# Performance work log

Hardware: AMD Instinct MI355X
Metric: run time of the kernel (lower is better)

## Reference

```python
import jax, jax.numpy as jnp
import numpy as np

L, B, T, V, E, H = 6, 4, 1024, 32000, 768, 12
D = E // H  # head_size = 64


def setup_inputs() -> dict:
    key = jax.random.key(0)
    ks = jax.random.split(key, 12)
    s = 0.02
    n = lambda k, shape: jax.random.normal(k, shape, jnp.float32) * s
    return {
        "idx": jax.random.randint(ks[0], (B, T), 0, V),
        "tok_emb": n(ks[1], (V, E)),
        "pos_emb": n(ks[2], (T, E)),
        "ln1_w": jnp.ones((L, E)), "ln1_b": jnp.zeros((L, E)),
        "wq": n(ks[3], (L, E, H, D)),
        "wk": n(ks[4], (L, E, H, D)),
        "wv": n(ks[5], (L, E, H, D)),
        "wo": n(ks[6], (L, E, E)), "bo": jnp.zeros((L, E)),
        "ln2_w": jnp.ones((L, E)), "ln2_b": jnp.zeros((L, E)),
        "w1": n(ks[7], (L, E, 4 * E)), "b1": jnp.zeros((L, 4 * E)),
        "w2": n(ks[8], (L, 4 * E, E)), "b2": jnp.zeros((L, E)),
        "lnf_w": jnp.ones((E,)), "lnf_b": jnp.zeros((E,)),
        "head_w": n(ks[9], (E, V)), "head_b": jnp.zeros((V,)),
    }


def _ln(x, w, b, eps=1e-5):
    m = x.mean(-1, keepdims=True)
    v = ((x - m) ** 2).mean(-1, keepdims=True)
    return (x - m) * jax.lax.rsqrt(v + eps) * w + b


def _forward(idx, tok_emb, pos_emb, ln1_w, ln1_b, wq, wk, wv, wo, bo,
             ln2_w, ln2_b, w1, b1, w2, b2, lnf_w, lnf_b, head_w, head_b):
    t = idx.shape[1]
    x = tok_emb[idx] + pos_emb[None, :t]          # [B,T,E]
    causal = jnp.tril(jnp.ones((t, t), bool))     # tril buffer
    scale = jnp.asarray(D, x.dtype) ** -0.5       # k.shape[-1] ** -0.5

    def block(x, p):
        l1w, l1b, Wq, Wk, Wv, Wo, Bo, l2w, l2b, W1, B1, W2, B2 = p
        h = _ln(x, l1w, l1b)
        q = jnp.einsum('btc,chd->bthd', h, Wq)
        k = jnp.einsum('btc,chd->bthd', h, Wk)
        v = jnp.einsum('btc,chd->bthd', h, Wv)
        wei = jnp.einsum('bqhd,bkhd->bhqk', q, k) * scale
        wei = jnp.where(causal, wei, -jnp.inf)
        wei = jax.nn.softmax(wei, axis=-1)
        att = jnp.einsum('bhqk,bkhd->bqhd', wei, v).reshape(x.shape)
        x = x + (att @ Wo + Bo)
        h2 = _ln(x, l2w, l2b)
        x = x + (jax.nn.relu(h2 @ W1 + B1) @ W2 + B2)
        return x, None

    params = (ln1_w, ln1_b, wq, wk, wv, wo, bo, ln2_w, ln2_b, w1, b1, w2, b2)
    x, _ = jax.lax.scan(block, x, params)
    x = _ln(x, lnf_w, lnf_b)
    return x @ head_w + head_b                    # [B,T,V] logits


def reference(idx, tok_emb, pos_emb, ln1_w, ln1_b, wq, wk, wv, wo, bo,
              ln2_w, ln2_b, w1, b1, w2, b2, lnf_w, lnf_b, head_w, head_b):
    return _forward(idx, tok_emb, pos_emb, ln1_w, ln1_b, wq, wk, wv, wo, bo,
                    ln2_w, ln2_b, w1, b1, w2, b2, lnf_w, lnf_b, head_w, head_b)
```

## Files before the change

kernel.cpp:

```cpp
#include <hip/hip_runtime.h>
#include <hip/hip_bf16.h>
#include <math.h>

#define L_LAYERS 6
#define BB 4
#define TT 1024
#define VV 32000
#define EE 768
#define HH 12
#define DD 64
#define BT (BB * TT)

typedef unsigned short u16;
typedef unsigned int   u32;
typedef __attribute__((ext_vector_type(8))) short short8;
typedef __attribute__((ext_vector_type(8))) unsigned short ushort8v;
typedef __attribute__((ext_vector_type(4))) unsigned short ushort4v;
typedef __attribute__((ext_vector_type(4))) float f32x4;

__device__ __forceinline__ float b2f_lo(u32 u) { union { u32 i; float f; } c; c.i = u << 16;          return c.f; }
__device__ __forceinline__ float b2f_hi(u32 u) { union { u32 i; float f; } c; c.i = u & 0xffff0000u;  return c.f; }
__device__ __forceinline__ u16  f2b(float f)   { union { float f; u32 i; } c{f}; u32 r = c.i + 0x7fffu + ((c.i >> 16) & 1u); return (u16)(r >> 16); }

__device__ __forceinline__ void gload16(const void* g, void* l) {
    __builtin_amdgcn_global_load_lds(
        (const __attribute__((address_space(1))) void*)g,
        (__attribute__((address_space(3))) void*)l, 16, 0, 0);
}

__global__ __launch_bounds__(256) void embed_kernel(
    const int* __restrict__ idx, const float* __restrict__ tok_emb,
    const float* __restrict__ pos_emb, float* __restrict__ x)
{
    int i = blockIdx.x * 256 + threadIdx.x;
    int e  = i % EE;
    int bt = i / EE;
    int t  = bt % TT;
    int tok = idx[bt];
    x[i] = tok_emb[(size_t)tok * EE + e] + pos_emb[(size_t)t * EE + e];
}

__global__ __launch_bounds__(256) void ln_kernel(
    const float* __restrict__ X, const float* __restrict__ w,
    const float* __restrict__ b, u16* __restrict__ Y)
{
    const int lane = threadIdx.x & 63;
    const size_t row = blockIdx.x * 4 + (threadIdx.x >> 6);
    const float* x = X + row * EE;

    f32x4 v[3];
    #pragma unroll
    for (int k = 0; k < 3; k++)
        v[k] = *(const f32x4*)&x[lane * 4 + k * 256];

    float s = 0.0f;
    #pragma unroll
    for (int k = 0; k < 3; k++) s += v[k][0] + v[k][1] + v[k][2] + v[k][3];
    #pragma unroll
    for (int off = 32; off; off >>= 1) s += __shfl_xor(s, off);
    const float mean = s * (1.0f / EE);

    float q = 0.0f;
    #pragma unroll
    for (int k = 0; k < 3; k++)
        #pragma unroll
        for (int j = 0; j < 4; j++) {
            v[k][j] -= mean;
            q += v[k][j] * v[k][j];
        }
    #pragma unroll
    for (int off = 32; off; off >>= 1) q += __shfl_xor(q, off);
    const float rstd = rsqrtf(q * (1.0f / EE) + 1e-5f);

    u16* y = Y + row * EE;
    #pragma unroll
    for (int k = 0; k < 3; k++) {
        const f32x4 wv = *(const f32x4*)&w[lane * 4 + k * 256];
        const f32x4 bv = *(const f32x4*)&b[lane * 4 + k * 256];
        ushort4v o;
        #pragma unroll
        for (int j = 0; j < 4; j++) o[j] = f2b(v[k][j] * rstd * wv[j] + bv[j]);
        *(ushort4v*)&y[lane * 4 + k * 256] = o;
    }
}

__device__ __forceinline__ void transpose_tile(
    const float* __restrict__ W, u16* __restrict__ Wt,
    int K, int N, int kt, int nt)
{
    __shared__ float t[32][33];
    const int k0 = kt * 32;
    const int n0 = nt * 32;
    const int c = threadIdx.x & 31;
    const int r = threadIdx.x >> 5;
    #pragma unroll
    for (int i = 0; i < 4; i++)
        t[r + i * 8][c] = W[(size_t)(k0 + r + i * 8) * N + n0 + c];
    __syncthreads();
    #pragma unroll
    for (int i = 0; i < 4; i++) {
        int rr = r + i * 8;
        Wt[(size_t)(n0 + rr) * K + k0 + c] = f2b(t[c][rr]);
    }
}

__global__ __launch_bounds__(256) void transpose_cvt(
    const float* __restrict__ W, u16* __restrict__ Wt, int K, int N)
{
    transpose_tile(W, Wt, K, N, blockIdx.y, blockIdx.x);
}

__global__ __launch_bounds__(256) void transpose_layer(
    const float* __restrict__ wq, const float* __restrict__ wk,
    const float* __restrict__ wv, const float* __restrict__ wo,
    const float* __restrict__ w1, const float* __restrict__ w2,
    u16* __restrict__ wt)
{
    const int t = blockIdx.x;
    if (t < 2304) {
        const int m = t / 576, r = t % 576;
        const float* Ws[4] = {wq, wk, wv, wo};
        transpose_tile(Ws[m], wt + (size_t)m * 768 * 768, 768, 768, r / 24, r % 24);
    } else if (t < 4608) {
        const int r = t - 2304;
        transpose_tile(w1, wt + (size_t)4 * 768 * 768, 768, 3072, r / 96, r % 96);
    } else {
        const int r = t - 4608;
        transpose_tile(w2, wt + (size_t)4 * 768 * 768 + (size_t)3072 * 768,
                       3072, 768, r / 24, r % 24);
    }
}

template<int RELU, int RES, int OUTBF, int MFRAG>
__global__ __launch_bounds__(256) void gemm_bf16(
    const u16* __restrict__ A, const u16* __restrict__ Bt,
    const float* __restrict__ bias, const float* __restrict__ res,
    void* __restrict__ Cv, int M, int N, int K)
{
    constexpr int TM = MFRAG * 32;
    __shared__ u16 As[TM * 64];
    __shared__ u16 Bs[128 * 64];

    const int tid  = threadIdx.x;
    const int lane = tid & 63;
    const int w    = tid >> 6;
    const int wr   = w >> 1, wc = w & 1;
    const int m0 = blockIdx.x * TM;
    const int n0 = blockIdx.y * 128;

    const int cs = (lane & 7) ^ (lane >> 3);
    const int rl = lane >> 3;

    int aoff[2 * MFRAG], boff[8];
    const int kq = lane >> 4;
    #pragma unroll
    for (int mi = 0; mi < MFRAG; mi++) {
        int rg = wr * (MFRAG * 16) + mi * 16 + (lane & 15);
        #pragma unroll
        for (int ks = 0; ks < 2; ks++)
            aoff[2 * mi + ks] = rg * 64 + (((ks * 4 + kq) ^ (rg & 7)) * 8);
    }
    #pragma unroll
    for (int ni = 0; ni < 4; ni++) {
        int rg = wc * 64 + ni * 16 + (lane & 15);
        #pragma unroll
        for (int ks = 0; ks < 2; ks++)
            boff[2 * ni + ks] = rg * 64 + (((ks * 4 + kq) ^ (rg & 7)) * 8);
    }

    f32x4 acc[MFRAG][4] = {};

    for (int k0 = 0; k0 < K; k0 += 64) {
        __syncthreads();
        #pragma unroll
        for (int i = 0; i < MFRAG; i++) {
            const int seg = i * 4 + w;
            const int row = seg * 8 + rl;
            gload16(A + (size_t)(m0 + row) * K + k0 + cs * 8, &As[seg * 512]);
        }
        #pragma unroll
        for (int i = 0; i < 4; i++) {
            const int seg = i * 4 + w;
            const int row = seg * 8 + rl;
            gload16(Bt + (size_t)(n0 + row) * K + k0 + cs * 8, &Bs[seg * 512]);
        }
        __syncthreads();
        #pragma unroll
        for (int ks = 0; ks < 2; ks++) {
            short8 af[MFRAG], bfv[4];
            #pragma unroll
            for (int mi = 0; mi < MFRAG; mi++) af[mi] = *(const short8*)&As[aoff[2 * mi + ks]];
            #pragma unroll
            for (int ni = 0; ni < 4; ni++) bfv[ni] = *(const short8*)&Bs[boff[2 * ni + ks]];
            #pragma unroll
            for (int mi = 0; mi < MFRAG; mi++)
                #pragma unroll
                for (int ni = 0; ni < 4; ni++)
                    acc[mi][ni] = __builtin_amdgcn_mfma_f32_16x16x32_bf16(
                        af[mi], bfv[ni], acc[mi][ni], 0, 0, 0);
        }
    }

    const int rbase = m0 + wr * (MFRAG * 16) + (lane >> 4) * 4;
    const int cbase = n0 + wc * 64 + (lane & 15);
    #pragma unroll
    for (int ni = 0; ni < 4; ni++) {
        const int c = cbase + ni * 16;
        const float bv = bias ? bias[c] : 0.0f;
        #pragma unroll
        for (int mi = 0; mi < MFRAG; mi++) {
            const int r = rbase + mi * 16;
            #pragma unroll
            for (int i = 0; i < 4; i++) {
                float v = acc[mi][ni][i] + bv;
                const size_t off = (size_t)(r + i) * N + c;
                if (RES)  v += res[off];
                if (RELU) v = fmaxf(v, 0.0f);
                if (OUTBF) ((u16*)Cv)[off] = f2b(v);
                else       ((float*)Cv)[off] = v;
            }
        }
    }
}

#define AST 72
__global__ __launch_bounds__(256) void attn_mfma(
    const u16* __restrict__ qkv, u16* __restrict__ O)
{
    const int tid = threadIdx.x;
    const int qi = blockIdx.x;
    const int h  = blockIdx.y;
    const int b  = blockIdx.z;
    const int q0 = qi * 64;

    __shared__ u16 Ks[2][64 * 64];
    __shared__ u16 Vt[2][80 * AST];
    __shared__ u16 Ps[64 * AST];

    const int lane = tid & 63;
    const int w    = tid >> 6;
    const int lr   = lane & 15;
    const int lk   = lane >> 4;

    const int cs = (lane & 7) ^ (lane >> 3);
    const int rl = lane >> 3;
    const int vk2 = tid & 31;
    const int vdc = tid >> 5;

    for (int i = tid; i < 16 * AST; i += 256) {
        const int r = i / AST, c = i % AST;
        const u16 v = (r == 0) ? (u16)0x3F80 : (u16)0;
        Vt[0][(64 + r) * AST + c] = v;
        Vt[1][(64 + r) * AST + c] = v;
    }

    {
        const int sr = tid >> 2, sc = tid & 3;
        const u16* src = qkv + (size_t)(b * TT + q0 + sr) * 2304 + h * 64 + sc * 16;
        *(ushort8v*)&Ps[sr * AST + sc * 16]     = *(const ushort8v*)src;
        *(ushort8v*)&Ps[sr * AST + sc * 16 + 8] = *(const ushort8v*)(src + 8);
    }
    __syncthreads();
    short8 aq[2];
    #pragma unroll
    for (int ks = 0; ks < 2; ks++)
        aq[ks] = *(const short8*)&Ps[(w * 16 + lr) * AST + lk * 8 + ks * 32];

    ushort8v vr0, vr1;
    auto K_ISSUE = [&](int t, int bf) {
        const int k0 = t * 64;
        #pragma unroll
        for (int j = 0; j < 2; ++j) {
            const int seg = j * 4 + w;
            const int row = seg * 8 + rl;
            gload16(qkv + (size_t)(b * TT + k0 + row) * 2304 + 768 + h * 64 + cs * 8,
                    &Ks[bf][seg * 512]);
        }
    };
    auto V_LOAD = [&](int t) {
        const int k0 = t * 64;
        const u16* p = qkv + (size_t)(b * TT + k0 + 2 * vk2) * 2304 + 1536 + h * 64 + vdc * 8;
        vr0 = *(const ushort8v*)p;
        vr1 = *(const ushort8v*)(p + 2304);
    };
    auto V_WRITE = [&](int bf) {
        #pragma unroll
        for (int j = 0; j < 8; ++j) {
            const u32 val = (u32)vr0[j] | ((u32)vr1[j] << 16);
            *(u32*)&Vt[bf][(vdc * 8 + j) * AST + 2 * vk2] = val;
        }
    };

    K_ISSUE(0, 0);
    V_LOAD(0);
    V_WRITE(0);
    __syncthreads();

    f32x4 oacc[5] = {};
    float m_run[4];
    #pragma unroll
    for (int i = 0; i < 4; i++) m_run[i] = -3.0e38f;

    const int qrow = q0 + w * 16 + lk * 4;
    const float SC = 0.18033688f;

    for (int t = 0; t <= qi; ++t) {
        const int cur = t & 1;

        f32x4 sfrag[4] = {};
        #pragma unroll
        for (int ks = 0; ks < 2; ks++)
            #pragma unroll
            for (int nt = 0; nt < 4; nt++) {
                const int rg = nt * 16 + lr;
                short8 bk = *(const short8*)&Ks[cur][rg * 64 + (((ks * 4 + lk) ^ (rg & 7)) * 8)];
                sfrag[nt] = __builtin_amdgcn_mfma_f32_16x16x32_bf16(aq[ks], bk, sfrag[nt], 0, 0, 0);
            }

        if (t < qi) { K_ISSUE(t + 1, cur ^ 1); V_LOAD(t + 1); }

        const int k0 = t * 64;
        float sv[4][4], mxv[4];
        float need = 0.0f;
        #pragma unroll
        for (int i = 0; i < 4; i++) {
            float mx = -3.0e38f;
            #pragma unroll
            for (int nt = 0; nt < 4; nt++) {
                float s = sfrag[nt][i] * SC;
                if (t == qi && (k0 + nt * 16 + lr) > (qrow + i)) s = -3.0e38f;
                sv[i][nt] = s;
                mx = fmaxf(mx, s);
            }
            mx = fmaxf(mx, __shfl_xor(mx, 1));
            mx = fmaxf(mx, __shfl_xor(mx, 2));
            mx = fmaxf(mx, __shfl_xor(mx, 4));
            mx = fmaxf(mx, __shfl_xor(mx, 8));
            mxv[i] = mx;
            need = fmaxf(need, mx - m_run[i]);
        }
        if (!__all(need <= 11.5f)) {
            #pragma unroll
            for (int i = 0; i < 4; i++) {
                const float m_new = fmaxf(m_run[i], mxv[i]);
                const float scale = exp2f(m_run[i] - m_new);
                #pragma unroll
                for (int dt = 0; dt < 5; dt++) oacc[dt][i] *= scale;
                m_run[i] = m_new;
            }
        }
        #pragma unroll
        for (int i = 0; i < 4; i++)
            #pragma unroll
            for (int nt = 0; nt < 4; nt++)
                sv[i][nt] = exp2f(sv[i][nt] - m_run[i]);

        #pragma unroll
        for (int i = 0; i < 4; i++)
            #pragma unroll
            for (int nt = 0; nt < 4; nt++)
                Ps[(w * 16 + lk * 4 + i) * AST + nt * 16 + lr] = f2b(sv[i][nt]);

        #pragma unroll
        for (int ks = 0; ks < 2; ks++) {
            short8 ap = *(const short8*)&Ps[(w * 16 + lr) * AST + lk * 8 + ks * 32];
            #pragma unroll
            for (int dt = 0; dt < 5; dt++) {
                short8 bv = *(const short8*)&Vt[cur][(dt * 16 + lr) * AST + lk * 8 + ks * 32];
                oacc[dt] = __builtin_amdgcn_mfma_f32_16x16x32_bf16(ap, bv, oacc[dt], 0, 0, 0);
            }
        }

        if (t < qi) V_WRITE(cur ^ 1);
        __syncthreads();
    }

    #pragma unroll
    for (int i = 0; i < 4; i++) {
        const float li  = __shfl(oacc[4][i], lane & 48);
        const float inv = 1.0f / li;
        u16* dst = O + (size_t)(b * TT + q0 + w * 16 + lk * 4 + i) * 768 + h * 64 + lr;
        #pragma unroll
        for (int dt = 0; dt < 4; dt++)
            dst[dt * 16] = f2b(oacc[dt][i] * inv);
    }
}

extern "C" void kernel_launch(void* const* d_in, const int* in_sizes, int n_in,
                              void* d_out, int out_size, void* d_ws, size_t ws_size,
                              hipStream_t stream)
{
    (void)in_sizes; (void)n_in; (void)out_size; (void)ws_size;

    const int*   idx     = (const int*)  d_in[0];
    const float* tok_emb = (const float*)d_in[1];
    const float* pos_emb = (const float*)d_in[2];
    const float* ln1_w   = (const float*)d_in[3];
    const float* ln1_b   = (const float*)d_in[4];
    const float* wq      = (const float*)d_in[5];
    const float* wk      = (const float*)d_in[6];
    const float* wv      = (const float*)d_in[7];
    const float* wo      = (const float*)d_in[8];
    const float* bo      = (const float*)d_in[9];
    const float* ln2_w   = (const float*)d_in[10];
    const float* ln2_b   = (const float*)d_in[11];
    const float* w1      = (const float*)d_in[12];
    const float* b1      = (const float*)d_in[13];
    const float* w2      = (const float*)d_in[14];
    const float* b2      = (const float*)d_in[15];
    const float* lnf_w   = (const float*)d_in[16];
    const float* lnf_b   = (const float*)d_in[17];
    const float* head_w  = (const float*)d_in[18];
    const float* head_b  = (const float*)d_in[19];
    float* out = (float*)d_out;

    const size_t S = (size_t)BT * EE;
    float* x   = (float*)d_ws;
    u16*  qkv  = (u16*)(x + S);
    u16*  hb   = qkv + (size_t)BT * 2304;
    u16*  ffh  = hb + S;
    u16*  wt   = ffh + (size_t)BT * 3072;

    embed_kernel<<<BT * EE / 256, 256, 0, stream>>>(idx, tok_emb, pos_emb, x);

    for (int l = 0; l < L_LAYERS; l++) {
        const size_t oE  = (size_t)l * EE;
        const size_t oEE = (size_t)l * EE * EE;
        const size_t oEF = (size_t)l * EE * 4 * EE;

        transpose_layer<<<6912, 256, 0, stream>>>(
            wq + oEE, wk + oEE, wv + oEE, wo + oEE, w1 + oEF, w2 + oEF, wt);

        ln_kernel<<<BT / 4, 256, 0, stream>>>(x, ln1_w + oE, ln1_b + oE, hb);
        gemm_bf16<0, 0, 1, 4><<<dim3(BT / 128, 2304 / 128), 256, 0, stream>>>(
            hb, wt, nullptr, nullptr, qkv, BT, 2304, 768);
        attn_mfma<<<dim3(TT / 64, HH, BB), 256, 0, stream>>>(qkv, hb);
        gemm_bf16<0, 1, 0, 2><<<dim3(BT / 64, 768 / 128), 256, 0, stream>>>(
            hb, wt + (size_t)3 * 768 * 768, bo + oE, x, x, BT, 768, 768);
        ln_kernel<<<BT / 4, 256, 0, stream>>>(x, ln2_w + oE, ln2_b + oE, hb);
        gemm_bf16<1, 0, 1, 4><<<dim3(BT / 128, 3072 / 128), 256, 0, stream>>>(
            hb, wt + (size_t)4 * 768 * 768, b1 + (size_t)l * 4 * EE, nullptr, ffh, BT, 3072, 768);
        gemm_bf16<0, 1, 0, 2><<<dim3(BT / 64, 768 / 128), 256, 0, stream>>>(
            ffh, wt + (size_t)4 * 768 * 768 + (size_t)3072 * 768, b2 + oE, x, x, BT, 768, 3072);
    }

    ln_kernel<<<BT / 4, 256, 0, stream>>>(x, lnf_w, lnf_b, hb);
    transpose_cvt<<<dim3(VV / 32, EE / 32), 256, 0, stream>>>(head_w, wt, EE, VV);
    gemm_bf16<0, 0, 0, 4><<<dim3(BT / 128, VV / 128), 256, 0, stream>>>(
        hb, wt, head_b, nullptr, out, BT, VV, 768);
}
```

Baseline: 1.425 ms.

## Batch all weight transposes into one launch and use nontemporal logits stores

When the workspace is large enough, all six layers' weights and the head weight are transposed and converted to bf16 in a single kernel launch up front, each into its own buffer, instead of one transpose launch per layer plus a separate head transpose. This removes seven small launches and lets the transpose work run with far more blocks in parallel. Non-residual fp32 GEMM outputs (the logits) are now written with nontemporal stores to avoid polluting the cache. The cost is a much larger workspace footprint, and the code falls back to the old per-layer path if the workspace is too small.

```diff
diff --git a/kernel.cpp b/kernel.cpp
--- a/kernel.cpp
+++ b/kernel.cpp
@@ -28,6 +28,9 @@
         (__attribute__((address_space(3))) void*)l, 16, 0, 0);
 }
 
+#define WT_LAYER 7077888u
+#define WT_HEAD_OFF ((size_t)L_LAYERS * WT_LAYER)
+
 __global__ __launch_bounds__(256) void embed_kernel(
     const int* __restrict__ idx, const float* __restrict__ tok_emb,
     const float* __restrict__ pos_emb, float* __restrict__ x)
@@ -104,19 +107,10 @@
     }
 }
 
-__global__ __launch_bounds__(256) void transpose_cvt(
-    const float* __restrict__ W, u16* __restrict__ Wt, int K, int N)
-{
-    transpose_tile(W, Wt, K, N, blockIdx.y, blockIdx.x);
-}
-
-__global__ __launch_bounds__(256) void transpose_layer(
-    const float* __restrict__ wq, const float* __restrict__ wk,
-    const float* __restrict__ wv, const float* __restrict__ wo,
-    const float* __restrict__ w1, const float* __restrict__ w2,
-    u16* __restrict__ wt)
-{
-    const int t = blockIdx.x;
+__device__ __forceinline__ void transpose_layer_core(
+    const float* wq, const float* wk, const float* wv, const float* wo,
+    const float* w1, const float* w2, u16* wt, int t)
+{
     if (t < 2304) {
         const int m = t / 576, r = t % 576;
         const float* Ws[4] = {wq, wk, wv, wo};
@@ -131,6 +125,41 @@
     }
 }
 
+__global__ __launch_bounds__(256) void transpose_layer(
+    const float* __restrict__ wq, const float* __restrict__ wk,
+    const float* __restrict__ wv, const float* __restrict__ wo,
+    const float* __restrict__ w1, const float* __restrict__ w2,
+    u16* __restrict__ wt)
+{
+    transpose_layer_core(wq, wk, wv, wo, w1, w2, wt, blockIdx.x);
+}
+
+__global__ __launch_bounds__(256) void transpose_cvt(
+    const float* __restrict__ W, u16* __restrict__ Wt, int K, int N)
+{
+    transpose_tile(W, Wt, K, N, blockIdx.y, blockIdx.x);
+}
+
+__global__ __launch_bounds__(256) void transpose_all(
+    const float* __restrict__ wq, const float* __restrict__ wk,
+    const float* __restrict__ wv, const float* __restrict__ wo,
+    const float* __restrict__ w1, const float* __restrict__ w2,
+    const float* __restrict__ head_w, u16* __restrict__ wt)
+{
+    const int t = blockIdx.x;
+    if (t < L_LAYERS * 6912) {
+        const int l = t / 6912, r = t % 6912;
+        const size_t oEE = (size_t)l * EE * EE;
+        const size_t oEF = (size_t)l * EE * 4 * EE;
+        transpose_layer_core(wq + oEE, wk + oEE, wv + oEE, wo + oEE,
+                             w1 + oEF, w2 + oEF,
+                             wt + (size_t)l * WT_LAYER, r);
+    } else {
+        const int r = t - L_LAYERS * 6912;
+        transpose_tile(head_w, wt + WT_HEAD_OFF, 768, 32000, r / 1000, r % 1000);
+    }
+}
+
 template<int RELU, int RES, int OUTBF, int MFRAG>
 __global__ __launch_bounds__(256) void gemm_bf16(
     const u16* __restrict__ A, const u16* __restrict__ Bt,
@@ -216,8 +245,13 @@
                 const size_t off = (size_t)(r + i) * N + c;
                 if (RES)  v += res[off];
                 if (RELU) v = fmaxf(v, 0.0f);
-                if (OUTBF) ((u16*)Cv)[off] = f2b(v);
-                else       ((float*)Cv)[off] = v;
+                if (OUTBF) {
+                    ((u16*)Cv)[off] = f2b(v);
+                } else if (!RES) {
+                    __builtin_nontemporal_store(v, &((float*)Cv)[off]);
+                } else {
+                    ((float*)Cv)[off] = v;
+                }
             }
         }
     }
@@ -390,7 +424,7 @@
                               void* d_out, int out_size, void* d_ws, size_t ws_size,
                               hipStream_t stream)
 {
-    (void)in_sizes; (void)n_in; (void)out_size; (void)ws_size;
+    (void)in_sizes; (void)n_in; (void)out_size;
 
     const int*   idx     = (const int*)  d_in[0];
     const float* tok_emb = (const float*)d_in[1];
@@ -421,31 +455,42 @@
     u16*  ffh  = hb + S;
     u16*  wt   = ffh + (size_t)BT * 3072;
 
+    const size_t need_big = 62914560u + 134086656u + 1024;
+    const bool big = (ws_size >= need_big);
+
     embed_kernel<<<BT * EE / 256, 256, 0, stream>>>(idx, tok_emb, pos_emb, x);
+
+    if (big)
+        transpose_all<<<L_LAYERS * 6912 + 24000, 256, 0, stream>>>(
+            wq, wk, wv, wo, w1, w2, head_w, wt);
 
     for (int l = 0; l < L_LAYERS; l++) {
         const size_t oE  = (size_t)l * EE;
         const size_t oEE = (size_t)l * EE * EE;
         const size_t oEF = (size_t)l * EE * 4 * EE;
-
-        transpose_layer<<<6912, 256, 0, stream>>>(
-            wq + oEE, wk + oEE, wv + oEE, wo + oEE, w1 + oEF, w2 + oEF, wt);
+        u16* wtl = big ? (wt + (size_t)l * WT_LAYER) : wt;
+
+        if (!big)
+            transpose_layer<<<6912, 256, 0, stream>>>(
+                wq + oEE, wk + oEE, wv + oEE, wo + oEE, w1 + oEF, w2 + oEF, wtl);
 
         ln_kernel<<<BT / 4, 256, 0, stream>>>(x, ln1_w + oE, ln1_b + oE, hb);
         gemm_bf16<0, 0, 1, 4><<<dim3(BT / 128, 2304 / 128), 256, 0, stream>>>(
-            hb, wt, nullptr, nullptr, qkv, BT, 2304, 768);
+            hb, wtl, nullptr, nullptr, qkv, BT, 2304, 768);
         attn_mfma<<<dim3(TT / 64, HH, BB), 256, 0, stream>>>(qkv, hb);
         gemm_bf16<0, 1, 0, 2><<<dim3(BT / 64, 768 / 128), 256, 0, stream>>>(
-            hb, wt + (size_t)3 * 768 * 768, bo + oE, x, x, BT, 768, 768);
+            hb, wtl + (size_t)3 * 768 * 768, bo + oE, x, x, BT, 768, 768);
         ln_kernel<<<BT / 4, 256, 0, stream>>>(x, ln2_w + oE, ln2_b + oE, hb);
         gemm_bf16<1, 0, 1, 4><<<dim3(BT / 128, 3072 / 128), 256, 0, stream>>>(
-            hb, wt + (size_t)4 * 768 * 768, b1 + (size_t)l * 4 * EE, nullptr, ffh, BT, 3072, 768);
+            hb, wtl + (size_t)4 * 768 * 768, b1 + (size_t)l * 4 * EE, nullptr, ffh, BT, 3072, 768);
         gemm_bf16<0, 1, 0, 2><<<dim3(BT / 64, 768 / 128), 256, 0, stream>>>(
-            ffh, wt + (size_t)4 * 768 * 768 + (size_t)3072 * 768, b2 + oE, x, x, BT, 768, 3072);
+            ffh, wtl + (size_t)4 * 768 * 768 + (size_t)3072 * 768, b2 + oE, x, x, BT, 768, 3072);
     }
 
     ln_kernel<<<BT / 4, 256, 0, stream>>>(x, lnf_w, lnf_b, hb);
-    transpose_cvt<<<dim3(VV / 32, EE / 32), 256, 0, stream>>>(head_w, wt, EE, VV);
+    u16* wth = big ? (wt + WT_HEAD_OFF) : wt;
+    if (!big)
+        transpose_cvt<<<dim3(VV / 32, EE / 32), 256, 0, stream>>>(head_w, wth, EE, VV);
     gemm_bf16<0, 0, 0, 4><<<dim3(BT / 128, VV / 128), 256, 0, stream>>>(
-        hb, wt, head_b, nullptr, out, BT, VV, 768);
-}
+        hb, wth, head_b, nullptr, out, BT, VV, 768);
+}
```

Result: no change. 1.416 ms (median of 2 runs) (-0.7%).
